# Kernel optimization log

Hardware: AMD Instinct MI355X
Metric: run time of the kernel (lower is better)

## Reference

```python
import jax, jax.numpy as jnp
import numpy as np

B, D = 4096, 512
STEPS = 50
LR, B1, B2, EPS = 0.01, 0.9, 0.999, 1e-8  # torch.optim.Adam defaults with lr=0.01


def setup_inputs() -> dict:
    key = jax.random.key(0)
    k1, k2, k3, k4 = jax.random.split(key, 4)
    s = jax.random.normal(k1, (B, D), dtype=jnp.float32)
    target_confidence = jax.random.uniform(k2, (B, 1), dtype=jnp.float32)
    # nn.Linear(style_dim, 1) init: U(-1/sqrt(D), 1/sqrt(D))
    lim = 1.0 / np.sqrt(D)
    W = jax.random.uniform(k3, (1, D), dtype=jnp.float32, minval=-lim, maxval=lim)
    b = jax.random.uniform(k4, (1,), dtype=jnp.float32, minval=-lim, maxval=lim)
    return {"s": s, "target_confidence": target_confidence, "W": W, "b": b}


def reference(s, target_confidence, W, b):
    # loss(x) = mse(sigmoid(x W^T + b), t) + l1(x, s); grad taken w.r.t. x only.
    def loss_fn(x):
        p = jax.nn.sigmoid(x @ W.T + b)                      # [B, 1]
        mse = jnp.mean((p - target_confidence) ** 2)
        d = x - s
        # stop_gradient(sign) so d|d|/dx = sign(d), with sign(0) = 0 (matches torch l1_loss subgradient)
        l1 = jnp.mean(jax.lax.stop_gradient(jnp.sign(d)) * d)
        return mse + l1

    grad_fn = jax.grad(loss_fn)

    def adam_step(carry, _):
        x, m, v, t = carry
        g = grad_fn(x)
        t = t + 1.0
        m = B1 * m + (1.0 - B1) * g
        v = B2 * v + (1.0 - B2) * g * g
        m_hat = m / (1.0 - B1 ** t)
        v_hat = v / (1.0 - B2 ** t)
        x = x - LR * m_hat / (jnp.sqrt(v_hat) + EPS)
        return (x, m, v, t), None

    init = (s, jnp.zeros_like(s), jnp.zeros_like(s), jnp.float32(0.0))
    (adjusted_s, _, _, _), _ = jax.lax.scan(adam_step, init, None, length=STEPS)
    return adjusted_s
```

## Files before the change

### kernel.cpp

```cpp
#include <hip/hip_runtime.h>

#define B_ 4096
#define D_ 512
#define STEPS_ 50

struct BcTab { float negA[STEPS_]; float u2[STEPS_]; };

#define DPP_ADD(x, ctrl) \
    ((x) + __int_as_float(__builtin_amdgcn_update_dpp( \
        0, __float_as_int(x), (ctrl), 0xf, 0xf, true)))

__device__ __forceinline__ float wave64_sum(float x) {
    x = DPP_ADD(x, 0x111);
    x = DPP_ADD(x, 0x112);
    x = DPP_ADD(x, 0x114);
    x = DPP_ADD(x, 0x118);
    x = DPP_ADD(x, 0x142);
    x = DPP_ADD(x, 0x143);
    return __int_as_float(__builtin_amdgcn_readlane(__float_as_int(x), 63));
}

__global__ __launch_bounds__(64, 1) void adam_rows_kernel(
    const float* __restrict__ s,
    const float* __restrict__ tgt,
    const float* __restrict__ W,
    const float* __restrict__ bias_p,
    float* __restrict__ out,
    const BcTab bc)
{
    const int lane = threadIdx.x;
    const int row  = blockIdx.x;

    const float4* srow4 = (const float4*)(s + (size_t)row * D_);
    const float4* W4    = (const float4*)W;

    float4 sa = srow4[lane];
    float4 sb = srow4[lane + 64];
    float4 wa = W4[lane];
    float4 wb = W4[lane + 64];
    const float t = tgt[row];

    float ss[8] = {sa.x, sa.y, sa.z, sa.w, sb.x, sb.y, sb.z, sb.w};
    float ws[8] = {wa.x, wa.y, wa.z, wa.w, wb.x, wb.y, wb.z, wb.w};
    float dl[8], M[8], V[8];

    const float c_mse = 2.0f / (float)B_;
    const unsigned c_l1_bits = 0x35000000u;

    float zdot = 0.0f;
#pragma unroll
    for (int k = 0; k < 8; ++k) zdot = fmaf(ss[k], ws[k], zdot);
    const float zb = wave64_sum(zdot) + bias_p[0];

    {
        const float p    = __builtin_amdgcn_rcpf(1.0f + __expf(-zb));
        const float coef = c_mse * (p - t) * p * (1.0f - p);
        const float negA = bc.negA[0];
        const float u2   = bc.u2[0];
#pragma unroll
        for (int k = 0; k < 8; ++k) {
            const float g = coef * ws[k];
            M[k] = g;
            V[k] = g * g;
            const float den = __builtin_amdgcn_sqrtf(V[k] * u2) + 1e-8f;
            dl[k] = (negA * M[k]) * __builtin_amdgcn_rcpf(den);
        }
    }

#pragma unroll 1
    for (int step = 1; step < STEPS_; ++step) {
        float dotd = 0.0f;
#pragma unroll
        for (int k = 0; k < 8; ++k) dotd = fmaf(dl[k], ws[k], dotd);
        const float z = zb + wave64_sum(dotd);

        const float p    = __builtin_amdgcn_rcpf(1.0f + __expf(-z));
        const float coef = c_mse * (p - t) * p * (1.0f - p);
        const float negA = bc.negA[step];
        const float u2   = bc.u2[step];

#pragma unroll
        for (int k = 0; k < 8; ++k) {
            const unsigned sbit = __float_as_uint(dl[k]) & 0x80000000u;
            const float gl1 = __uint_as_float(sbit | c_l1_bits);
            const float g = fmaf(coef, ws[k], gl1);
            M[k] = fmaf(0.9f,   M[k], g);
            V[k] = fmaf(0.999f, V[k], g * g);
            const float den = __builtin_amdgcn_sqrtf(V[k] * u2) + 1e-8f;
            dl[k] = fmaf(negA * M[k], __builtin_amdgcn_rcpf(den), dl[k]);
        }
    }

    float4 oa = {ss[0] + dl[0], ss[1] + dl[1], ss[2] + dl[2], ss[3] + dl[3]};
    float4 ob = {ss[4] + dl[4], ss[5] + dl[5], ss[6] + dl[6], ss[7] + dl[7]};
    float4* orow4 = (float4*)(out + (size_t)row * D_);
    orow4[lane]      = oa;
    orow4[lane + 64] = ob;
}

extern "C" void kernel_launch(void* const* d_in, const int* in_sizes, int n_in,
                              void* d_out, int out_size, void* d_ws, size_t ws_size,
                              hipStream_t stream) {
    const float* s    = (const float*)d_in[0];
    const float* tgt  = (const float*)d_in[1];
    const float* W    = (const float*)d_in[2];
    const float* bias = (const float*)d_in[3];
    float* out = (float*)d_out;

    BcTab bc;
    double p1 = 1.0, p2 = 1.0;
    for (int t = 0; t < STEPS_; ++t) {
        p1 *= 0.9; p2 *= 0.999;
        bc.negA[t] = (float)(-0.001 / (1.0 - p1));
        bc.u2[t]   = (float)( 0.001 / (1.0 - p2));
    }

    adam_rows_kernel<<<dim3(B_), dim3(64), 0, stream>>>(s, tgt, W, bias, out, bc);
}
```

Before: 100.3 us.

## Process two rows per wave and fold bias correction into a single rsqrt scale

Each 64-lane block now handles two rows, so the two independent reductions and update chains interleave and hide each other's DPP and transcendental latency. The eps term is dropped and sqrt+rcp becomes a single rsq with the bias-correction factors combined into one host-computed scale. W is prescaled by the MSE factor, and the next step's dot product is accumulated inside the update loop, removing a separate pass. The risks are small numerical deviations from ignoring eps, and halving the block count to 2048 single-wave blocks, which lowers the number of waves available to the GPU.

New measurement: 96.66 us. -3.6%, faster.

```diff
diff --git a/kernel.cpp b/kernel.cpp
--- a/kernel.cpp
+++ b/kernel.cpp
@@ -4,7 +4,7 @@
 #define D_ 512
 #define STEPS_ 50
 
-struct BcTab { float negA[STEPS_]; float u2[STEPS_]; };
+struct BcTab { float An[STEPS_]; };
 
 #define DPP_ADD(x, ctrl) \
     ((x) + __int_as_float(__builtin_amdgcn_update_dpp( \
@@ -20,6 +20,16 @@
     return __int_as_float(__builtin_amdgcn_readlane(__float_as_int(x), 63));
 }
 
+__device__ __forceinline__ float sgn_l1(float d) {
+    return __uint_as_float((__float_as_uint(d) & 0x80000000u) | 0x35000000u);
+}
+
+__device__ __forceinline__ float coef_from_z(float z, float t) {
+    const float e = __expf(-z);
+    const float q = __builtin_amdgcn_rcpf(1.0f + e);
+    return (q - t) * (e * (q * q));
+}
+
 __global__ __launch_bounds__(64, 1) void adam_rows_kernel(
     const float* __restrict__ s,
     const float* __restrict__ tgt,
@@ -29,73 +39,119 @@
     const BcTab bc)
 {
     const int lane = threadIdx.x;
-    const int row  = blockIdx.x;
+    const int r0 = blockIdx.x * 2;
+    const int r1 = r0 + 1;
 
-    const float4* srow4 = (const float4*)(s + (size_t)row * D_);
-    const float4* W4    = (const float4*)W;
+    const float4* s0 = (const float4*)(s + (size_t)r0 * D_);
+    const float4* s1 = (const float4*)(s + (size_t)r1 * D_);
+    const float4* W4 = (const float4*)W;
 
-    float4 sa = srow4[lane];
-    float4 sb = srow4[lane + 64];
-    float4 wa = W4[lane];
-    float4 wb = W4[lane + 64];
-    const float t = tgt[row];
-
-    float ss[8] = {sa.x, sa.y, sa.z, sa.w, sb.x, sb.y, sb.z, sb.w};
-    float ws[8] = {wa.x, wa.y, wa.z, wa.w, wb.x, wb.y, wb.z, wb.w};
-    float dl[8], M[8], V[8];
+    float4 sa0 = s0[lane], sb0 = s0[lane + 64];
+    float4 sa1 = s1[lane], sb1 = s1[lane + 64];
+    float4 wa  = W4[lane], wb  = W4[lane + 64];
+    const float t0 = tgt[r0], t1 = tgt[r1];
+    const float b  = bias_p[0];
 
     const float c_mse = 2.0f / (float)B_;
-    const unsigned c_l1_bits = 0x35000000u;
+    const float K     = (float)B_ * 0.5f;
 
-    float zdot = 0.0f;
+    float2 ws[4] = {{wa.x * c_mse, wa.y * c_mse}, {wa.z * c_mse, wa.w * c_mse},
+                    {wb.x * c_mse, wb.y * c_mse}, {wb.z * c_mse, wb.w * c_mse}};
+    float2 ss0[4] = {{sa0.x, sa0.y}, {sa0.z, sa0.w}, {sb0.x, sb0.y}, {sb0.z, sb0.w}};
+    float2 ss1[4] = {{sa1.x, sa1.y}, {sa1.z, sa1.w}, {sb1.x, sb1.y}, {sb1.z, sb1.w}};
+    float2 dl0[4], dl1[4], M0[4], M1[4], V0[4], V1[4];
+
+    float za0 = 0.0f, za1 = 0.0f;
 #pragma unroll
-    for (int k = 0; k < 8; ++k) zdot = fmaf(ss[k], ws[k], zdot);
-    const float zb = wave64_sum(zdot) + bias_p[0];
+    for (int j = 0; j < 4; ++j) {
+        za0 = fmaf(ss0[j].x, ws[j].x, za0); za0 = fmaf(ss0[j].y, ws[j].y, za0);
+        za1 = fmaf(ss1[j].x, ws[j].x, za1); za1 = fmaf(ss1[j].y, ws[j].y, za1);
+    }
+    const float zb0 = fmaf(K, wave64_sum(za0), b);
+    const float zb1 = fmaf(K, wave64_sum(za1), b);
+
+    float du0, du1;
 
     {
-        const float p    = __builtin_amdgcn_rcpf(1.0f + __expf(-zb));
-        const float coef = c_mse * (p - t) * p * (1.0f - p);
-        const float negA = bc.negA[0];
-        const float u2   = bc.u2[0];
+        const float c0 = coef_from_z(zb0, t0);
+        const float c1 = coef_from_z(zb1, t1);
+        const float An = bc.An[0];
+        float a0 = 0.0f, a1 = 0.0f;
 #pragma unroll
-        for (int k = 0; k < 8; ++k) {
-            const float g = coef * ws[k];
-            M[k] = g;
-            V[k] = g * g;
-            const float den = __builtin_amdgcn_sqrtf(V[k] * u2) + 1e-8f;
-            dl[k] = (negA * M[k]) * __builtin_amdgcn_rcpf(den);
+        for (int j = 0; j < 4; ++j) {
+#pragma unroll
+            for (int h = 0; h < 2; ++h) {
+                float* w_  = h ? &ws[j].y  : &ws[j].x;
+                float* m0_ = h ? &M0[j].y  : &M0[j].x;
+                float* v0_ = h ? &V0[j].y  : &V0[j].x;
+                float* d0_ = h ? &dl0[j].y : &dl0[j].x;
+                float* m1_ = h ? &M1[j].y  : &M1[j].x;
+                float* v1_ = h ? &V1[j].y  : &V1[j].x;
+                float* d1_ = h ? &dl1[j].y : &dl1[j].x;
+                const float g0 = c0 * *w_;
+                const float g1 = c1 * *w_;
+                *m0_ = g0; *v0_ = g0 * g0;
+                *m1_ = g1; *v1_ = g1 * g1;
+                const float r0r = __builtin_amdgcn_rsqf(fmaxf(*v0_, 1e-37f));
+                const float r1r = __builtin_amdgcn_rsqf(fmaxf(*v1_, 1e-37f));
+                *d0_ = (An * *m0_) * r0r;
+                *d1_ = (An * *m1_) * r1r;
+                a0 = fmaf(*d0_, *w_, a0);
+                a1 = fmaf(*d1_, *w_, a1);
+            }
         }
+        du0 = a0; du1 = a1;
     }
 
 #pragma unroll 1
     for (int step = 1; step < STEPS_; ++step) {
-        float dotd = 0.0f;
+        const float z0 = fmaf(K, wave64_sum(du0), zb0);
+        const float z1 = fmaf(K, wave64_sum(du1), zb1);
+        const float c0 = coef_from_z(z0, t0);
+        const float c1 = coef_from_z(z1, t1);
+        const float An = bc.An[step];
+
+        float a0 = 0.0f, a1 = 0.0f;
 #pragma unroll
-        for (int k = 0; k < 8; ++k) dotd = fmaf(dl[k], ws[k], dotd);
-        const float z = zb + wave64_sum(dotd);
-
-        const float p    = __builtin_amdgcn_rcpf(1.0f + __expf(-z));
-        const float coef = c_mse * (p - t) * p * (1.0f - p);
-        const float negA = bc.negA[step];
-        const float u2   = bc.u2[step];
-
+        for (int j = 0; j < 4; ++j) {
 #pragma unroll
-        for (int k = 0; k < 8; ++k) {
-            const unsigned sbit = __float_as_uint(dl[k]) & 0x80000000u;
-            const float gl1 = __uint_as_float(sbit | c_l1_bits);
-            const float g = fmaf(coef, ws[k], gl1);
-            M[k] = fmaf(0.9f,   M[k], g);
-            V[k] = fmaf(0.999f, V[k], g * g);
-            const float den = __builtin_amdgcn_sqrtf(V[k] * u2) + 1e-8f;
-            dl[k] = fmaf(negA * M[k], __builtin_amdgcn_rcpf(den), dl[k]);
+            for (int h = 0; h < 2; ++h) {
+                float* w_  = h ? &ws[j].y  : &ws[j].x;
+                float* m0_ = h ? &M0[j].y  : &M0[j].x;
+                float* v0_ = h ? &V0[j].y  : &V0[j].x;
+                float* d0_ = h ? &dl0[j].y : &dl0[j].x;
+                float* m1_ = h ? &M1[j].y  : &M1[j].x;
+                float* v1_ = h ? &V1[j].y  : &V1[j].x;
+                float* d1_ = h ? &dl1[j].y : &dl1[j].x;
+                const float g0 = fmaf(c0, *w_, sgn_l1(*d0_));
+                const float g1 = fmaf(c1, *w_, sgn_l1(*d1_));
+                *m0_ = fmaf(0.9f, *m0_, g0);
+                *m1_ = fmaf(0.9f, *m1_, g1);
+                *v0_ = fmaf(0.999f, *v0_, g0 * g0);
+                *v1_ = fmaf(0.999f, *v1_, g1 * g1);
+                const float r0r = __builtin_amdgcn_rsqf(fmaxf(*v0_, 1e-37f));
+                const float r1r = __builtin_amdgcn_rsqf(fmaxf(*v1_, 1e-37f));
+                *d0_ = fmaf(An * *m0_, r0r, *d0_);
+                *d1_ = fmaf(An * *m1_, r1r, *d1_);
+                a0 = fmaf(*d0_, *w_, a0);
+                a1 = fmaf(*d1_, *w_, a1);
+            }
         }
+        du0 = a0; du1 = a1;
     }
 
-    float4 oa = {ss[0] + dl[0], ss[1] + dl[1], ss[2] + dl[2], ss[3] + dl[3]};
-    float4 ob = {ss[4] + dl[4], ss[5] + dl[5], ss[6] + dl[6], ss[7] + dl[7]};
-    float4* orow4 = (float4*)(out + (size_t)row * D_);
-    orow4[lane]      = oa;
-    orow4[lane + 64] = ob;
+    float4 oa0 = {ss0[0].x + dl0[0].x, ss0[0].y + dl0[0].y,
+                  ss0[1].x + dl0[1].x, ss0[1].y + dl0[1].y};
+    float4 ob0 = {ss0[2].x + dl0[2].x, ss0[2].y + dl0[2].y,
+                  ss0[3].x + dl0[3].x, ss0[3].y + dl0[3].y};
+    float4 oa1 = {ss1[0].x + dl1[0].x, ss1[0].y + dl1[0].y,
+                  ss1[1].x + dl1[1].x, ss1[1].y + dl1[1].y};
+    float4 ob1 = {ss1[2].x + dl1[2].x, ss1[2].y + dl1[2].y,
+                  ss1[3].x + dl1[3].x, ss1[3].y + dl1[3].y};
+    float4* o0 = (float4*)(out + (size_t)r0 * D_);
+    float4* o1 = (float4*)(out + (size_t)r1 * D_);
+    o0[lane] = oa0; o0[lane + 64] = ob0;
+    o1[lane] = oa1; o1[lane + 64] = ob1;
 }
 
 extern "C" void kernel_launch(void* const* d_in, const int* in_sizes, int n_in,
@@ -111,9 +167,9 @@
     double p1 = 1.0, p2 = 1.0;
     for (int t = 0; t < STEPS_; ++t) {
         p1 *= 0.9; p2 *= 0.999;
-        bc.negA[t] = (float)(-0.001 / (1.0 - p1));
-        bc.u2[t]   = (float)( 0.001 / (1.0 - p2));
+        bc.An[t] = (float)((-0.001 / (1.0 - p1)) /
+                           __builtin_sqrt(0.001 / (1.0 - p2)));
     }
 
-    adam_rows_kernel<<<dim3(B_), dim3(64), 0, stream>>>(s, tgt, W, bias, out, bc);
+    adam_rows_kernel<<<dim3(B_ / 2), dim3(64), 0, stream>>>(s, tgt, W, bias, out, bc);
 }
```

## Process four rows per wave with staggered reductions and rsqrt-based Adam update

Applied to the files above, without the earlier changes.

Each wave now handles four rows and interleaves their serial 50-step chains, so one row's cross-lane reduction and sigmoid latency can overlap with the other rows' elementwise updates. The bias-correction table moves from a host-built kernel argument into per-lane values computed on the device and read out with readlane. The Adam denominator is rewritten as a single rsqrt with rescaled constants (weights pre-scaled by 2/B), dropping the separate sqrt, add-epsilon and reciprocal. This changes how epsilon enters the update (a tiny 1e-30 floor inside V instead of adding 1e-8 to the square root), which may shift numerics slightly. It also cuts the grid to 1024 waves, which lowers occupancy and parallelism across CUs.

New measurement: 92.50 us. 7.8% less time.

```diff
diff --git a/kernel.cpp b/kernel.cpp
--- a/kernel.cpp
+++ b/kernel.cpp
@@ -3,8 +3,6 @@
 #define B_ 4096
 #define D_ 512
 #define STEPS_ 50
-
-struct BcTab { float negA[STEPS_]; float u2[STEPS_]; };
 
 #define DPP_ADD(x, ctrl) \
     ((x) + __int_as_float(__builtin_amdgcn_update_dpp( \
@@ -20,82 +18,118 @@
     return __int_as_float(__builtin_amdgcn_readlane(__float_as_int(x), 63));
 }
 
+__device__ __forceinline__ float coef_from_z(float z, float t) {
+    const float e = __expf(-z);
+    const float q = __builtin_amdgcn_rcpf(1.0f + e);
+    return (q - t) * (e * (q * q));
+}
+
 __global__ __launch_bounds__(64, 1) void adam_rows_kernel(
     const float* __restrict__ s,
     const float* __restrict__ tgt,
     const float* __restrict__ W,
     const float* __restrict__ bias_p,
-    float* __restrict__ out,
-    const BcTab bc)
+    float* __restrict__ out)
 {
     const int lane = threadIdx.x;
-    const int row  = blockIdx.x;
+    const int rb = blockIdx.x * 4;
 
-    const float4* srow4 = (const float4*)(s + (size_t)row * D_);
-    const float4* W4    = (const float4*)W;
+    float vAn;
+    {
+        const float t1 = (float)(lane + 1);
+        const float p1 = exp2f(t1 * -0.15200309344505f);
+        const float p2 = exp2f(t1 * -0.00144345345258f);
+        vAn = (-0.0316227766017f * __builtin_amdgcn_sqrtf(1.0f - p2)) *
+              __builtin_amdgcn_rcpf(1.0f - p1);
+    }
 
-    float4 sa = srow4[lane];
-    float4 sb = srow4[lane + 64];
-    float4 wa = W4[lane];
-    float4 wb = W4[lane + 64];
-    const float t = tgt[row];
+    const float4* W4 = (const float4*)W;
+    const float4 wa = W4[lane], wb = W4[lane + 64];
+    const float b = bias_p[0];
 
-    float ss[8] = {sa.x, sa.y, sa.z, sa.w, sb.x, sb.y, sb.z, sb.w};
-    float ws[8] = {wa.x, wa.y, wa.z, wa.w, wb.x, wb.y, wb.z, wb.w};
-    float dl[8], M[8], V[8];
+    const float c_mse = 0x1p-11f;
+    const float K     = 2048.0f;
+    const float c_l1  = 0x1p-21f;
 
-    const float c_mse = 2.0f / (float)B_;
-    const unsigned c_l1_bits = 0x35000000u;
+    float ws[8] = {wa.x * c_mse, wa.y * c_mse, wa.z * c_mse, wa.w * c_mse,
+                   wb.x * c_mse, wb.y * c_mse, wb.z * c_mse, wb.w * c_mse};
 
-    float zdot = 0.0f;
+    float M[4][8], V[4][8], dl[4][8];
+    float du[4], zb[4], tg[4], c[4];
+
 #pragma unroll
-    for (int k = 0; k < 8; ++k) zdot = fmaf(ss[k], ws[k], zdot);
-    const float zb = wave64_sum(zdot) + bias_p[0];
+    for (int r = 0; r < 4; ++r) {
+        const float4* sr = (const float4*)(s + (size_t)(rb + r) * D_);
+        const float4 sa = sr[lane], sb = sr[lane + 64];
+        tg[r] = tgt[rb + r];
+        const float e[8] = {sa.x, sa.y, sa.z, sa.w, sb.x, sb.y, sb.z, sb.w};
+        float za = 0.0f;
+#pragma unroll
+        for (int k = 0; k < 8; ++k) za = fmaf(e[k], ws[k], za);
+        zb[r] = fmaf(K, wave64_sum(za), b);
+    }
 
     {
-        const float p    = __builtin_amdgcn_rcpf(1.0f + __expf(-zb));
-        const float coef = c_mse * (p - t) * p * (1.0f - p);
-        const float negA = bc.negA[0];
-        const float u2   = bc.u2[0];
+        const float An0 =
+            __int_as_float(__builtin_amdgcn_readlane(__float_as_int(vAn), 0));
 #pragma unroll
-        for (int k = 0; k < 8; ++k) {
-            const float g = coef * ws[k];
-            M[k] = g;
-            V[k] = g * g;
-            const float den = __builtin_amdgcn_sqrtf(V[k] * u2) + 1e-8f;
-            dl[k] = (negA * M[k]) * __builtin_amdgcn_rcpf(den);
+        for (int r = 0; r < 4; ++r) {
+            const float cr = coef_from_z(zb[r], tg[r]);
+            float a = 0.0f;
+#pragma unroll
+            for (int k = 0; k < 8; ++k) {
+                const float g = cr * ws[k];
+                M[r][k] = g;
+                V[r][k] = fmaf(g, g, 1e-30f);
+                dl[r][k] = (An0 * g) * __builtin_amdgcn_rsqf(V[r][k]);
+                a = fmaf(dl[r][k], ws[k], a);
+            }
+            du[r] = a;
         }
     }
 
+    c[0] = coef_from_z(fmaf(K, wave64_sum(du[0]), zb[0]), tg[0]);
+    c[1] = coef_from_z(fmaf(K, wave64_sum(du[1]), zb[1]), tg[1]);
+    c[2] = coef_from_z(fmaf(K, wave64_sum(du[2]), zb[2]), tg[2]);
+
 #pragma unroll 1
     for (int step = 1; step < STEPS_; ++step) {
-        float dotd = 0.0f;
-#pragma unroll
-        for (int k = 0; k < 8; ++k) dotd = fmaf(dl[k], ws[k], dotd);
-        const float z = zb + wave64_sum(dotd);
+        const float An =
+            __int_as_float(__builtin_amdgcn_readlane(__float_as_int(vAn), step));
 
-        const float p    = __builtin_amdgcn_rcpf(1.0f + __expf(-z));
-        const float coef = c_mse * (p - t) * p * (1.0f - p);
-        const float negA = bc.negA[step];
-        const float u2   = bc.u2[step];
+        c[3] = coef_from_z(fmaf(K, wave64_sum(du[3]), zb[3]), tg[3]);
 
 #pragma unroll
-        for (int k = 0; k < 8; ++k) {
-            const unsigned sbit = __float_as_uint(dl[k]) & 0x80000000u;
-            const float gl1 = __uint_as_float(sbit | c_l1_bits);
-            const float g = fmaf(coef, ws[k], gl1);
-            M[k] = fmaf(0.9f,   M[k], g);
-            V[k] = fmaf(0.999f, V[k], g * g);
-            const float den = __builtin_amdgcn_sqrtf(V[k] * u2) + 1e-8f;
-            dl[k] = fmaf(negA * M[k], __builtin_amdgcn_rcpf(den), dl[k]);
+        for (int r = 0; r < 4; ++r) {
+            float a = 0.0f;
+#pragma unroll
+            for (int k = 0; k < 8; ++k) {
+                const float g =
+                    fmaf(c[r], ws[k], __builtin_copysignf(c_l1, dl[r][k]));
+                M[r][k] = fmaf(0.9f,   M[r][k], g);
+                V[r][k] = fmaf(0.999f, V[r][k], g * g);
+                dl[r][k] =
+                    fmaf(An * M[r][k], __builtin_amdgcn_rsqf(V[r][k]), dl[r][k]);
+                a = fmaf(dl[r][k], ws[k], a);
+            }
+            du[r] = a;
+            if (r != 3)
+                c[r] = coef_from_z(fmaf(K, wave64_sum(a), zb[r]), tg[r]);
         }
     }
 
-    float4 oa = {ss[0] + dl[0], ss[1] + dl[1], ss[2] + dl[2], ss[3] + dl[3]};
-    float4 ob = {ss[4] + dl[4], ss[5] + dl[5], ss[6] + dl[6], ss[7] + dl[7]};
-    float4* orow4 = (float4*)(out + (size_t)row * D_);
-    orow4[lane]      = oa;
-    orow4[lane + 64] = ob;
+#pragma unroll
+    for (int r = 0; r < 4; ++r) {
+        const float4* sr = (const float4*)(s + (size_t)(rb + r) * D_);
+        const float4 sa = sr[lane], sb = sr[lane + 64];
+        float4 oa = {sa.x + dl[r][0], sa.y + dl[r][1],
+                     sa.z + dl[r][2], sa.w + dl[r][3]};
+        float4 ob = {sb.x + dl[r][4], sb.y + dl[r][5],
+                     sb.z + dl[r][6], sb.w + dl[r][7]};
+        float4* orow = (float4*)(out + (size_t)(rb + r) * D_);
+        orow[lane]      = oa;
+        orow[lane + 64] = ob;
+    }
 }
 
 extern "C" void kernel_launch(void* const* d_in, const int* in_sizes, int n_in,
@@ -107,13 +141,5 @@
     const float* bias = (const float*)d_in[3];
     float* out = (float*)d_out;
 
-    BcTab bc;
-    double p1 = 1.0, p2 = 1.0;
-    for (int t = 0; t < STEPS_; ++t) {
-        p1 *= 0.9; p2 *= 0.999;
-        bc.negA[t] = (float)(-0.001 / (1.0 - p1));
-        bc.u2[t]   = (float)( 0.001 / (1.0 - p2));
-    }
-
-    adam_rows_kernel<<<dim3(B_), dim3(64), 0, stream>>>(s, tgt, W, bias, out, bc);
+    adam_rows_kernel<<<dim3(B_ / 4), dim3(64), 0, stream>>>(s, tgt, W, bias, out);
 }
```
